# Performance work log

Measured on AMD Instinct MI355X. Metric: run time of the kernel, lower is better.

Reference implementation:

```python
import jax, jax.numpy as jnp
import numpy as np

NUM_HEADS = 6
KEY_DIM = 16
D_HEAD = 32  # attn_ratio(2) * key_dim(16)


def conv1x1_bn(x, W, scale, bias):
    # 1x1 conv (no bias) + folded BatchNorm (eval mode) as per-channel affine.
    y = jnp.einsum('oi,bihw->bohw', W, x)
    return y * scale[None, :, None, None] + bias[None, :, None, None]


def setup_inputs() -> dict:
    key = jax.random.key(0)
    ks = jax.random.split(key, 16)
    B, C, H, W = 4, 384, 48, 48
    dim_s = C // 4  # 96
    nh_kd = NUM_HEADS * KEY_DIM  # 96
    dh = NUM_HEADS * D_HEAD      # 192

    def w(k, o, i):
        return jax.random.normal(k, (o, i), dtype=jnp.float32) / np.sqrt(i)

    return {
        'xx': jax.random.normal(ks[0], (B, C, H, W), dtype=jnp.float32),
        'Wq': w(ks[1], nh_kd, dim_s),
        'q_scale': jax.random.uniform(ks[2], (nh_kd,), dtype=jnp.float32, minval=0.5, maxval=1.5),
        'q_bias': 0.1 * jax.random.normal(ks[3], (nh_kd,), dtype=jnp.float32),
        'Wk': w(ks[4], nh_kd, C),
        'k_scale': jax.random.uniform(ks[5], (nh_kd,), dtype=jnp.float32, minval=0.5, maxval=1.5),
        'k_bias': 0.1 * jax.random.normal(ks[6], (nh_kd,), dtype=jnp.float32),
        'Wv': w(ks[7], dh, C),
        'v_scale': jax.random.uniform(ks[8], (dh,), dtype=jnp.float32, minval=0.5, maxval=1.5),
        'v_bias': 0.1 * jax.random.normal(ks[9], (dh,), dtype=jnp.float32),
        'Wp': w(ks[10], dim_s, dh),
        'p_scale': jax.random.uniform(ks[11], (dim_s,), dtype=jnp.float32, minval=0.5, maxval=1.5),
        'p_bias': 0.1 * jax.random.normal(ks[12], (dim_s,), dtype=jnp.float32),
        'Wo': w(ks[13], C, dim_s),
        'o_scale': jax.random.uniform(ks[14], (C,), dtype=jnp.float32, minval=0.5, maxval=1.5),
        'o_bias': 0.1 * jax.random.normal(ks[15], (C,), dtype=jnp.float32),
    }


def reference(xx, Wq, q_scale, q_bias, Wk, k_scale, k_bias, Wv, v_scale, v_bias,
              Wp, p_scale, p_bias, Wo, o_scale, o_bias):
    B, C, H, W = xx.shape
    dim_s = C // 4
    N = H * W
    x = xx[:, 3 * dim_s:]  # last channel split -> query stream [B, dim_s, H, W]

    q = conv1x1_bn(x, Wq, q_scale, q_bias)                    # [B, nh_kd, H, W]
    q = q.reshape(B, NUM_HEADS, KEY_DIM, N).transpose(0, 1, 3, 2)  # [B,h,N,kd]
    k = conv1x1_bn(xx, Wk, k_scale, k_bias).reshape(B, NUM_HEADS, KEY_DIM, N)  # [B,h,kd,N]
    v = conv1x1_bn(xx, Wv, v_scale, v_bias).reshape(B, NUM_HEADS, D_HEAD, N)   # [B,h,d,N]

    # NOTE: original forward never applies key_dim**-0.5 scaling -- faithful to that.
    attn = jax.nn.softmax(jnp.einsum('bhnk,bhkm->bhnm', q, k), axis=-1)  # [B,h,N,N]
    out = jnp.einsum('bhnm,bhdm->bhdn', attn, v)                         # [B,h,d,N]
    out = out.reshape(B, NUM_HEADS * D_HEAD, H, W)

    out = conv1x1_bn(jax.nn.relu(out), Wp, p_scale, p_bias)  # [B, dim_s, H, W]
    xres = x + out  # drop_path=0 -> identity
    y = jax.nn.relu(conv1x1_bn(xres, Wo, o_scale, o_bias))   # [B, C, H, W]
    return y
```

## Files before the change

kernel.cpp:

```cpp
#include <hip/hip_runtime.h>
#include <hip/hip_bf16.h>
#include <math.h>

#define BB 4
#define CIN 384
#define NHD 6
#define KDIM 16
#define DHEAD 32
#define NPOS 2304
#define DIMS 96
#define DHTOT 192

constexpr size_t AL(size_t x) { return (x + 255) & ~(size_t)255; }
constexpr size_t B_SC1 = 0;
constexpr size_t B_BS1 = B_SC1 + 384 * 4;
constexpr size_t B_SC2 = B_BS1 + 384 * 4;
constexpr size_t B_BS2 = B_SC2 + 96 * 4;
constexpr size_t B_SC3 = B_BS2 + 96 * 4;
constexpr size_t B_BS3 = B_SC3 + 384 * 4;
constexpr size_t B_W1  = AL(B_BS3 + 384 * 4);
constexpr size_t B_W2  = AL(B_W1 + (size_t)384 * 384 * 2);
constexpr size_t B_W3  = AL(B_W2 + (size_t)96 * 192 * 2);
constexpr size_t B_XH  = AL(B_W3 + (size_t)384 * 96 * 2);
constexpr size_t B_XL  = AL(B_XH + (size_t)BB * NPOS * CIN * 2);
constexpr size_t B_Q   = AL(B_XL + (size_t)BB * NPOS * CIN * 2);
constexpr size_t B_K   = AL(B_Q + (size_t)BB * NHD * NPOS * KDIM * 2);
constexpr size_t B_V   = AL(B_K + (size_t)BB * NHD * NPOS * KDIM * 2);
constexpr size_t B_OP  = AL(B_V + (size_t)BB * NHD * DHEAD * NPOS * 2);
constexpr size_t B_MP  = AL(B_OP + (size_t)2 * BB * DHTOT * NPOS * 4);
constexpr size_t B_LP  = AL(B_MP + (size_t)2 * 24 * NPOS * 4);
constexpr size_t B_OBT = AL(B_LP + (size_t)2 * 24 * NPOS * 4);
constexpr size_t B_XRT = AL(B_OBT + (size_t)BB * NPOS * DHTOT * 2);

#define WS_F(off) ((float*)((char*)ws + (off)))
#define WS_U(off) ((ushort*)((char*)ws + (off)))

typedef __attribute__((ext_vector_type(8))) short bf16x8;
typedef __attribute__((ext_vector_type(16))) float f32x16;
typedef __attribute__((ext_vector_type(2))) int int2v;

__device__ inline ushort f2bf(float f) {
    __hip_bfloat16 h = __float2bfloat16(f);
    return *reinterpret_cast<ushort*>(&h);
}
__device__ inline float bf2f(ushort u) {
    uint x = (uint)u << 16;
    return __uint_as_float(x);
}
__device__ inline float exp2_fast(float x) {
    float r;
    asm volatile("v_exp_f32 %0, %1" : "=v"(r) : "v"(x));
    return r;
}
__device__ inline uint cvt_pk_bf16(float lo, float hi) {
    uint r;
    asm volatile("v_cvt_pk_bf16_f32 %0, %1, %2" : "=v"(r) : "v"(lo), "v"(hi));
    return r;
}
__device__ inline void phswap(uint& a, uint& b) {
    int2v r = __builtin_amdgcn_permlane32_swap((int)a, (int)b, false, false);
    a = (uint)r[0]; b = (uint)r[1];
}
__device__ inline float xhalf_max(float x) {
    uint a = __float_as_uint(x), b = a;
    phswap(a, b);
    return fmaxf(__uint_as_float(a), __uint_as_float(b));
}
__device__ inline float xhalf_add(float x) {
    uint a = __float_as_uint(x), b = a;
    phswap(a, b);
    return __uint_as_float(a) + __uint_as_float(b);
}

#define MFMA32(A, B, C) __builtin_amdgcn_mfma_f32_32x32x16_bf16(A, B, C, 0, 0, 0)
#define LOG2E 1.4426950408889634f

__global__ void prep_kernel(const float* Wq, const float* qs, const float* qb,
                            const float* Wk, const float* ks, const float* kb,
                            const float* Wv, const float* vs, const float* vb,
                            const float* Wp, const float* ps, const float* pb,
                            const float* Wo, const float* os_, const float* ob,
                            float* ws) {
    ushort* W1 = WS_U(B_W1);
    ushort* W2 = WS_U(B_W2);
    ushort* W3 = WS_U(B_W3);
    int idx = blockIdx.x * blockDim.x + threadIdx.x;
    int stride = gridDim.x * blockDim.x;
    for (int t = idx; t < 384 * 384; t += stride) {
        int o = t / 384, i = t % 384;
        float v;
        if (o < 96)       v = (i >= 288) ? Wq[o * 96 + (i - 288)] : 0.f;
        else if (o < 192) v = Wk[(o - 96) * 384 + i];
        else              v = Wv[(o - 192) * 384 + i];
        W1[t] = f2bf(v);
    }
    for (int t = idx; t < 96 * 192; t += stride) W2[t] = f2bf(Wp[t]);
    for (int t = idx; t < 384 * 96; t += stride) W3[t] = f2bf(Wo[t]);
    if (idx < 384) {
        float s, bv;
        if (idx < 96)       { s = qs[idx] * LOG2E; bv = qb[idx] * LOG2E; }
        else if (idx < 192) { s = ks[idx - 96];    bv = kb[idx - 96]; }
        else                { s = vs[idx - 192];   bv = vb[idx - 192]; }
        WS_F(B_SC1)[idx] = s;    WS_F(B_BS1)[idx] = bv;
        WS_F(B_SC3)[idx] = os_[idx]; WS_F(B_BS3)[idx] = ob[idx];
    }
    if (idx < 96) { WS_F(B_SC2)[idx] = ps[idx]; WS_F(B_BS2)[idx] = pb[idx]; }
}

__global__ __launch_bounds__(256) void xcvt(const float* __restrict__ xx, float* ws) {
    ushort* Xh = WS_U(B_XH);
    ushort* Xl = WS_U(B_XL);
    int nt = blockIdx.x, it = blockIdx.y, b = blockIdx.z;
    __shared__ ushort tileH[64][66];
    __shared__ ushort tileL[64][66];
    int t = threadIdx.x;
    int ir = t >> 4, nc = (t & 15) * 4;
    const float* src = xx + ((size_t)b * CIN + it * 64) * NPOS + nt * 64;
#pragma unroll
    for (int ii = 0; ii < 64; ii += 16) {
        float4 v = *(const float4*)&src[(size_t)(ii + ir) * NPOS + nc];
        float vv[4] = {v.x, v.y, v.z, v.w};
#pragma unroll
        for (int j = 0; j < 4; ++j) {
            ushort h = f2bf(vv[j]);
            tileH[ii + ir][nc + j] = h;
            tileL[ii + ir][nc + j] = f2bf(vv[j] - bf2f(h));
        }
    }
    __syncthreads();
    int nl = t >> 2, i16 = (t & 3) * 16;
    ushort tmpH[16], tmpL[16];
#pragma unroll
    for (int j = 0; j < 16; ++j) { tmpH[j] = tileH[i16 + j][nl]; tmpL[j] = tileL[i16 + j][nl]; }
    size_t doff = ((size_t)b * NPOS + nt * 64 + nl) * CIN + it * 64 + i16;
    *(bf16x8*)&Xh[doff]     = *(bf16x8*)&tmpH[0];
    *(bf16x8*)&Xh[doff + 8] = *(bf16x8*)&tmpH[8];
    *(bf16x8*)&Xl[doff]     = *(bf16x8*)&tmpL[0];
    *(bf16x8*)&Xl[doff + 8] = *(bf16x8*)&tmpL[8];
}

__global__ __launch_bounds__(256) void qkv_mfma(float* ws) {
    const ushort* W1 = WS_U(B_W1);
    const ushort* Xh = WS_U(B_XH);
    const ushort* Xl = WS_U(B_XL);
    const float* sc1 = WS_F(B_SC1);
    const float* bs1 = WS_F(B_BS1);
    ushort* Qb = WS_U(B_Q);
    ushort* Kb = WS_U(B_K);
    ushort* Vt = WS_U(B_V);

    int nt = blockIdx.x, ot = blockIdx.y, b = blockIdx.z;
    int wave = threadIdx.x >> 6, lane = threadIdx.x & 63;
    int l31 = lane & 31, hl = lane >> 5;
    int obase = ot * 64 + (wave >> 1) * 32;
    int nbase = nt * 64 + (wave & 1) * 32;

    const ushort* arow  = W1 + (size_t)(obase + l31) * CIN + hl * 8;
    size_t boff = ((size_t)b * NPOS + nbase + l31) * CIN + hl * 8;
    const ushort* browh = Xh + boff;
    f32x16 acc = {};
#pragma unroll
    for (int k0 = 0; k0 < 384; k0 += 16)
        acc = MFMA32(*(const bf16x8*)(arow + k0), *(const bf16x8*)(browh + k0), acc);
    if (obase < 192) {
        const ushort* browl = Xl + boff;
#pragma unroll
        for (int k0 = 0; k0 < 384; k0 += 16)
            acc = MFMA32(*(const bf16x8*)(arow + k0), *(const bf16x8*)(browl + k0), acc);
    }

    int n = nbase + l31;
    if (obase < 96) {
#pragma unroll
        for (int r = 0; r < 16; ++r) {
            int o = obase + (r & 3) + 8 * (r >> 2) + 4 * hl;
            float v = acc[r] * sc1[o] + bs1[o];
            int h = o >> 4, kk = o & 15;
            Qb[((size_t)(b * NHD + h) * NPOS + n) * KDIM + kk] = f2bf(v);
        }
    } else if (obase < 192) {
#pragma unroll
        for (int r = 0; r < 16; ++r) {
            int o = obase + (r & 3) + 8 * (r >> 2) + 4 * hl;
            float v = acc[r] * sc1[o] + bs1[o];
            int oo = o - 96;
            int h = oo >> 4, kk = oo & 15;
            Kb[((size_t)(b * NHD + h) * NPOS + n) * KDIM + kk] = f2bf(v);
        }
    } else {
#pragma unroll
        for (int r = 0; r < 16; ++r) {
            int o = obase + (r & 3) + 8 * (r >> 2) + 4 * hl;
            float v = acc[r] * sc1[o] + bs1[o];
            int oo = o - 192;
            int d = oo & 31, hh = oo >> 5;
            Vt[((size_t)(b * NHD + hh) * DHEAD + d) * NPOS + n] = f2bf(v);
        }
    }
}

__global__ __launch_bounds__(256) void attn_mfma(float* ws) {
    const ushort* Qb = WS_U(B_Q);
    const ushort* Kb = WS_U(B_K);
    const ushort* Vt = WS_U(B_V);
    float* Op = WS_F(B_OP);
    float* Mp = WS_F(B_MP);
    float* Lp = WS_F(B_LP);

    int qt = blockIdx.x;
    int bh = blockIdx.y;
    int ms = blockIdx.z;
    int wave = threadIdx.x >> 6, lane = threadIdx.x & 63;
    int l31 = lane & 31, hl = lane >> 5;
    int n0 = qt * 128 + wave * 32;
    int n = n0 + l31;

    bf16x8 qf = *(const bf16x8*)(Qb + ((size_t)bh * NPOS + n) * KDIM + hl * 8);
    const ushort* kbase = Kb + (size_t)bh * NPOS * KDIM;
    const ushort* vbase = Vt + (size_t)bh * DHEAD * NPOS + (size_t)l31 * NPOS;

    f32x16 oacc = (f32x16)0.0f;
    float m_run = -1e30f, l_run = 0.f;

    int mend = ms * 1152 + 1152;
    for (int m0 = ms * 1152; m0 < mend; m0 += 32) {
        bf16x8 kf = *(const bf16x8*)(kbase + (size_t)(m0 + l31) * KDIM + hl * 8);
        f32x16 s = MFMA32(kf, qf, (f32x16)0.0f);

        float pm = s[0];
#pragma unroll
        for (int r = 1; r < 16; ++r) pm = fmaxf(pm, s[r]);
        pm = xhalf_max(pm);

        if (__any(pm > m_run + 8.f)) {
            float newm = fmaxf(m_run, pm);
            float sc = exp2_fast(m_run - newm);
#pragma unroll
            for (int r = 0; r < 16; ++r) oacc[r] *= sc;
            l_run *= sc;
            m_run = newm;
        }

        float p[16], psum = 0.f;
#pragma unroll
        for (int r = 0; r < 16; ++r) { p[r] = exp2_fast(s[r] - m_run); psum += p[r]; }
        l_run += xhalf_add(psum);

        uint w[8];
#pragma unroll
        for (int j = 0; j < 8; ++j) w[j] = cvt_pk_bf16(p[2 * j], p[2 * j + 1]);
        phswap(w[0], w[2]);
        phswap(w[1], w[3]);
        phswap(w[4], w[6]);
        phswap(w[5], w[7]);

        bf16x8 pb0, pb1;
        ((uint*)&pb0)[0] = w[0]; ((uint*)&pb0)[1] = w[1];
        ((uint*)&pb0)[2] = w[2]; ((uint*)&pb0)[3] = w[3];
        ((uint*)&pb1)[0] = w[4]; ((uint*)&pb1)[1] = w[5];
        ((uint*)&pb1)[2] = w[6]; ((uint*)&pb1)[3] = w[7];

        bf16x8 va0 = *(const bf16x8*)(vbase + m0 + hl * 8);
        bf16x8 va1 = *(const bf16x8*)(vbase + m0 + 16 + hl * 8);
        oacc = MFMA32(va0, pb0, oacc);
        oacc = MFMA32(va1, pb1, oacc);
    }

    int b = bh / NHD, h = bh % NHD;
    float* obase = Op + ((size_t)(ms * BB + b) * DHTOT + h * DHEAD) * NPOS + n;
#pragma unroll
    for (int r = 0; r < 16; ++r) {
        int d = (r & 3) + 8 * (r >> 2) + 4 * hl;
        obase[(size_t)d * NPOS] = oacc[r];
    }
    Mp[(size_t)(ms * 24 + bh) * NPOS + n] = m_run;
    Lp[(size_t)(ms * 24 + bh) * NPOS + n] = l_run;
}

__global__ __launch_bounds__(256) void attn_combine(float* ws) {
    const float* Op = WS_F(B_OP);
    const float* Mp = WS_F(B_MP);
    const float* Lp = WS_F(B_LP);
    ushort* Obt = WS_U(B_OBT);

    int idx = blockIdx.x * 256 + threadIdx.x;
    int bh = idx / NPOS, n = idx % NPOS;
    int b = bh / NHD, h = bh % NHD;

    float m0 = Mp[(size_t)bh * NPOS + n];
    float m1 = Mp[(size_t)(24 + bh) * NPOS + n];
    float l0 = Lp[(size_t)bh * NPOS + n];
    float l1 = Lp[(size_t)(24 + bh) * NPOS + n];
    float gm = fmaxf(m0, m1);
    float w0 = exp2_fast(m0 - gm), w1 = exp2_fast(m1 - gm);
    float inv = 1.f / (l0 * w0 + l1 * w1);
    w0 *= inv; w1 *= inv;

    const float* p0 = Op + ((size_t)b * DHTOT + h * DHEAD) * NPOS + n;
    const float* p1 = Op + ((size_t)(BB + b) * DHTOT + h * DHEAD) * NPOS + n;
    ushort tmp[32];
#pragma unroll
    for (int d = 0; d < 32; ++d) {
        float v = p0[(size_t)d * NPOS] * w0 + p1[(size_t)d * NPOS] * w1;
        tmp[d] = f2bf(fmaxf(v, 0.f));
    }
    ushort* dst = Obt + ((size_t)b * NPOS + n) * DHTOT + h * DHEAD;
#pragma unroll
    for (int c = 0; c < 4; ++c) *(bf16x8*)&dst[c * 8] = *(bf16x8*)&tmp[c * 8];
}

__global__ __launch_bounds__(256) void pproj_mfma(const float* __restrict__ xx, float* ws) {
    const ushort* W2 = WS_U(B_W2);
    const ushort* Obt = WS_U(B_OBT);
    const float* sc2 = WS_F(B_SC2);
    const float* bs2 = WS_F(B_BS2);
    ushort* XRt = WS_U(B_XRT);

    int nt = blockIdx.x, ot = blockIdx.y, b = blockIdx.z;
    int wave = threadIdx.x >> 6, lane = threadIdx.x & 63;
    int l31 = lane & 31, hl = lane >> 5;
    int obase = ot * 32;
    int nbase = nt * 128 + wave * 32;

    const ushort* arow = W2 + (size_t)(obase + l31) * DHTOT + hl * 8;
    const ushort* brow = Obt + ((size_t)b * NPOS + nbase + l31) * DHTOT + hl * 8;
    f32x16 acc = {};
#pragma unroll
    for (int k0 = 0; k0 < 192; k0 += 16)
        acc = MFMA32(*(const bf16x8*)(arow + k0), *(const bf16x8*)(brow + k0), acc);

    int n = nbase + l31;
#pragma unroll
    for (int r = 0; r < 16; ++r) {
        int o = obase + (r & 3) + 8 * (r >> 2) + 4 * hl;
        float v = acc[r] * sc2[o] + bs2[o] + xx[((size_t)b * CIN + 288 + o) * NPOS + n];
        XRt[((size_t)b * NPOS + n) * DIMS + o] = f2bf(v);
    }
}

__global__ __launch_bounds__(256) void oproj_mfma(float* ws, float* __restrict__ y) {
    const ushort* W3 = WS_U(B_W3);
    const ushort* XRt = WS_U(B_XRT);
    const float* sc3 = WS_F(B_SC3);
    const float* bs3 = WS_F(B_BS3);

    int nt = blockIdx.x, ot = blockIdx.y, b = blockIdx.z;
    int wave = threadIdx.x >> 6, lane = threadIdx.x & 63;
    int l31 = lane & 31, hl = lane >> 5;
    int obase = ot * 64 + (wave >> 1) * 32;
    int nbase = nt * 64 + (wave & 1) * 32;

    const ushort* arow = W3 + (size_t)(obase + l31) * DIMS + hl * 8;
    const ushort* brow = XRt + ((size_t)b * NPOS + nbase + l31) * DIMS + hl * 8;
    f32x16 acc = {};
#pragma unroll
    for (int k0 = 0; k0 < 96; k0 += 16)
        acc = MFMA32(*(const bf16x8*)(arow + k0), *(const bf16x8*)(brow + k0), acc);

    int n = nbase + l31;
#pragma unroll
    for (int r = 0; r < 16; ++r) {
        int o = obase + (r & 3) + 8 * (r >> 2) + 4 * hl;
        float v = fmaxf(acc[r] * sc3[o] + bs3[o], 0.f);
        y[((size_t)b * CIN + o) * NPOS + n] = v;
    }
}

extern "C" void kernel_launch(void* const* d_in, const int* in_sizes, int n_in,
                              void* d_out, int out_size, void* d_ws, size_t ws_size,
                              hipStream_t stream) {
    const float* xx = (const float*)d_in[0];
    const float* Wq = (const float*)d_in[1];
    const float* qs = (const float*)d_in[2];
    const float* qb = (const float*)d_in[3];
    const float* Wk = (const float*)d_in[4];
    const float* ks = (const float*)d_in[5];
    const float* kb = (const float*)d_in[6];
    const float* Wv = (const float*)d_in[7];
    const float* vs = (const float*)d_in[8];
    const float* vb = (const float*)d_in[9];
    const float* Wp = (const float*)d_in[10];
    const float* ps = (const float*)d_in[11];
    const float* pb = (const float*)d_in[12];
    const float* Wo = (const float*)d_in[13];
    const float* os_ = (const float*)d_in[14];
    const float* ob = (const float*)d_in[15];
    float* ws = (float*)d_ws;
    float* y = (float*)d_out;

    prep_kernel<<<256, 256, 0, stream>>>(Wq, qs, qb, Wk, ks, kb, Wv, vs, vb,
                                         Wp, ps, pb, Wo, os_, ob, ws);
    xcvt<<<dim3(36, 6, BB), 256, 0, stream>>>(xx, ws);
    qkv_mfma<<<dim3(36, 6, BB), 256, 0, stream>>>(ws);
    attn_mfma<<<dim3(18, 24, 2), 256, 0, stream>>>(ws);
    attn_combine<<<216, 256, 0, stream>>>(ws);
    pproj_mfma<<<dim3(18, 3, BB), 256, 0, stream>>>(xx, ws);
    oproj_mfma<<<dim3(36, 6, BB), 256, 0, stream>>>(ws, y);
}
```

Baseline: 207.4 us.

## Split attention keys four ways, fuse prep into x conversion, vectorize Q/K stores

Raises the attention key-split factor from 2 to 4, so the grid grows to 1728 blocks and the combine kernel merges four partial results. Weight preparation moves into the x-conversion kernel, removing one launch. Q/K epilogue writes become packed 4-element stores, and the max and sum reductions are rebalanced into trees to shorten dependency chains. The price is larger partial-output buffers and more combine-stage traffic.

Result: no change. 204.2 us (-1.5%).

```diff
diff --git a/kernel.cpp b/kernel.cpp
--- a/kernel.cpp
+++ b/kernel.cpp
@@ -10,6 +10,7 @@
 #define NPOS 2304
 #define DIMS 96
 #define DHTOT 192
+#define MS 4
 
 constexpr size_t AL(size_t x) { return (x + 255) & ~(size_t)255; }
 constexpr size_t B_SC1 = 0;
@@ -27,9 +28,9 @@
 constexpr size_t B_K   = AL(B_Q + (size_t)BB * NHD * NPOS * KDIM * 2);
 constexpr size_t B_V   = AL(B_K + (size_t)BB * NHD * NPOS * KDIM * 2);
 constexpr size_t B_OP  = AL(B_V + (size_t)BB * NHD * DHEAD * NPOS * 2);
-constexpr size_t B_MP  = AL(B_OP + (size_t)2 * BB * DHTOT * NPOS * 4);
-constexpr size_t B_LP  = AL(B_MP + (size_t)2 * 24 * NPOS * 4);
-constexpr size_t B_OBT = AL(B_LP + (size_t)2 * 24 * NPOS * 4);
+constexpr size_t B_MP  = AL(B_OP + (size_t)MS * BB * DHTOT * NPOS * 4);
+constexpr size_t B_LP  = AL(B_MP + (size_t)MS * 24 * NPOS * 4);
+constexpr size_t B_OBT = AL(B_LP + (size_t)MS * 24 * NPOS * 4);
 constexpr size_t B_XRT = AL(B_OBT + (size_t)BB * NPOS * DHTOT * 2);
 
 #define WS_F(off) ((float*)((char*)ws + (off)))
@@ -57,6 +58,9 @@
     asm volatile("v_cvt_pk_bf16_f32 %0, %1, %2" : "=v"(r) : "v"(lo), "v"(hi));
     return r;
 }
+__device__ inline float fmax3(float a, float b, float c) {
+    return fmaxf(fmaxf(a, b), c);
+}
 __device__ inline void phswap(uint& a, uint& b) {
     int2v r = __builtin_amdgcn_permlane32_swap((int)a, (int)b, false, false);
     a = (uint)r[0]; b = (uint)r[1];
@@ -75,39 +79,13 @@
 #define MFMA32(A, B, C) __builtin_amdgcn_mfma_f32_32x32x16_bf16(A, B, C, 0, 0, 0)
 #define LOG2E 1.4426950408889634f
 
-__global__ void prep_kernel(const float* Wq, const float* qs, const float* qb,
+__global__ __launch_bounds__(256) void setup_kernel(const float* __restrict__ xx,
+                            const float* Wq, const float* qs, const float* qb,
                             const float* Wk, const float* ks, const float* kb,
                             const float* Wv, const float* vs, const float* vb,
                             const float* Wp, const float* ps, const float* pb,
                             const float* Wo, const float* os_, const float* ob,
                             float* ws) {
-    ushort* W1 = WS_U(B_W1);
-    ushort* W2 = WS_U(B_W2);
-    ushort* W3 = WS_U(B_W3);
-    int idx = blockIdx.x * blockDim.x + threadIdx.x;
-    int stride = gridDim.x * blockDim.x;
-    for (int t = idx; t < 384 * 384; t += stride) {
-        int o = t / 384, i = t % 384;
-        float v;
-        if (o < 96)       v = (i >= 288) ? Wq[o * 96 + (i - 288)] : 0.f;
-        else if (o < 192) v = Wk[(o - 96) * 384 + i];
-        else              v = Wv[(o - 192) * 384 + i];
-        W1[t] = f2bf(v);
-    }
-    for (int t = idx; t < 96 * 192; t += stride) W2[t] = f2bf(Wp[t]);
-    for (int t = idx; t < 384 * 96; t += stride) W3[t] = f2bf(Wo[t]);
-    if (idx < 384) {
-        float s, bv;
-        if (idx < 96)       { s = qs[idx] * LOG2E; bv = qb[idx] * LOG2E; }
-        else if (idx < 192) { s = ks[idx - 96];    bv = kb[idx - 96]; }
-        else                { s = vs[idx - 192];   bv = vb[idx - 192]; }
-        WS_F(B_SC1)[idx] = s;    WS_F(B_BS1)[idx] = bv;
-        WS_F(B_SC3)[idx] = os_[idx]; WS_F(B_BS3)[idx] = ob[idx];
-    }
-    if (idx < 96) { WS_F(B_SC2)[idx] = ps[idx]; WS_F(B_BS2)[idx] = pb[idx]; }
-}
-
-__global__ __launch_bounds__(256) void xcvt(const float* __restrict__ xx, float* ws) {
     ushort* Xh = WS_U(B_XH);
     ushort* Xl = WS_U(B_XL);
     int nt = blockIdx.x, it = blockIdx.y, b = blockIdx.z;
@@ -137,6 +115,35 @@
     *(bf16x8*)&Xh[doff + 8] = *(bf16x8*)&tmpH[8];
     *(bf16x8*)&Xl[doff]     = *(bf16x8*)&tmpL[0];
     *(bf16x8*)&Xl[doff + 8] = *(bf16x8*)&tmpL[8];
+
+    ushort* W1 = WS_U(B_W1);
+    ushort* W2 = WS_U(B_W2);
+    ushort* W3 = WS_U(B_W3);
+    int gid = (blockIdx.z * gridDim.y + blockIdx.y) * gridDim.x + blockIdx.x;
+    int idx = gid * 256 + t;
+    int stride = gridDim.x * gridDim.y * gridDim.z * 256;
+    for (int u = idx; u < 384 * 384; u += stride) {
+        int o = u / 384, i = u % 384;
+        float v;
+        if (o < 96)       v = (i >= 288) ? Wq[o * 96 + (i - 288)] : 0.f;
+        else if (o < 192) v = Wk[(o - 96) * 384 + i];
+        else              v = Wv[(o - 192) * 384 + i];
+        W1[u] = f2bf(v);
+    }
+    for (int u = idx; u < 96 * 192; u += stride) W2[u] = f2bf(Wp[u]);
+    for (int u = idx; u < 384 * 96; u += stride) W3[u] = f2bf(Wo[u]);
+    if (idx < 384) {
+        float s, bv;
+        if (idx < 96)       { s = qs[idx] * LOG2E; bv = qb[idx] * LOG2E; }
+        else if (idx < 192) { s = ks[idx - 96];    bv = kb[idx - 96]; }
+        else                { s = vs[idx - 192];   bv = vb[idx - 192]; }
+        WS_F(B_SC1)[idx] = s;    WS_F(B_BS1)[idx] = bv;
+        WS_F(B_SC3)[idx] = os_[idx]; WS_F(B_BS3)[idx] = ob[idx];
+    }
+    if (idx >= 256 * 256 && idx < 256 * 256 + 96) {
+        int j = idx - 256 * 256;
+        WS_F(B_SC2)[j] = ps[j]; WS_F(B_BS2)[j] = pb[j];
+    }
 }
 
 __global__ __launch_bounds__(256) void qkv_mfma(float* ws) {
@@ -170,22 +177,20 @@
     }
 
     int n = nbase + l31;
-    if (obase < 96) {
-#pragma unroll
-        for (int r = 0; r < 16; ++r) {
-            int o = obase + (r & 3) + 8 * (r >> 2) + 4 * hl;
-            float v = acc[r] * sc1[o] + bs1[o];
-            int h = o >> 4, kk = o & 15;
-            Qb[((size_t)(b * NHD + h) * NPOS + n) * KDIM + kk] = f2bf(v);
-        }
-    } else if (obase < 192) {
-#pragma unroll
-        for (int r = 0; r < 16; ++r) {
-            int o = obase + (r & 3) + 8 * (r >> 2) + 4 * hl;
-            float v = acc[r] * sc1[o] + bs1[o];
-            int oo = o - 96;
-            int h = oo >> 4, kk = oo & 15;
-            Kb[((size_t)(b * NHD + h) * NPOS + n) * KDIM + kk] = f2bf(v);
+    if (obase < 192) {
+        ushort* dst = (obase < 96) ? Qb : Kb;
+        int ob2 = (obase < 96) ? obase : obase - 96;
+#pragma unroll
+        for (int g = 0; g < 4; ++g) {
+            int od = ob2 + 8 * g + 4 * hl;
+            ushort4 pk;
+            float v0 = acc[4 * g + 0] * sc1[obase + 8 * g + 4 * hl + 0] + bs1[obase + 8 * g + 4 * hl + 0];
+            float v1 = acc[4 * g + 1] * sc1[obase + 8 * g + 4 * hl + 1] + bs1[obase + 8 * g + 4 * hl + 1];
+            float v2 = acc[4 * g + 2] * sc1[obase + 8 * g + 4 * hl + 2] + bs1[obase + 8 * g + 4 * hl + 2];
+            float v3 = acc[4 * g + 3] * sc1[obase + 8 * g + 4 * hl + 3] + bs1[obase + 8 * g + 4 * hl + 3];
+            pk.x = f2bf(v0); pk.y = f2bf(v1); pk.z = f2bf(v2); pk.w = f2bf(v3);
+            int h = od >> 4, kk = od & 15;
+            *(ushort4*)&dst[((size_t)(b * NHD + h) * NPOS + n) * KDIM + kk] = pk;
         }
     } else {
 #pragma unroll
@@ -222,14 +227,18 @@
     f32x16 oacc = (f32x16)0.0f;
     float m_run = -1e30f, l_run = 0.f;
 
-    int mend = ms * 1152 + 1152;
-    for (int m0 = ms * 1152; m0 < mend; m0 += 32) {
+    const int span = NPOS / MS;
+    int mstart = ms * span, mend = mstart + span;
+    for (int m0 = mstart; m0 < mend; m0 += 32) {
         bf16x8 kf = *(const bf16x8*)(kbase + (size_t)(m0 + l31) * KDIM + hl * 8);
         f32x16 s = MFMA32(kf, qf, (f32x16)0.0f);
 
-        float pm = s[0];
-#pragma unroll
-        for (int r = 1; r < 16; ++r) pm = fmaxf(pm, s[r]);
+        float t0 = fmax3(s[0], s[1], s[2]);
+        float t1 = fmax3(s[3], s[4], s[5]);
+        float t2 = fmax3(s[6], s[7], s[8]);
+        float t3 = fmax3(s[9], s[10], s[11]);
+        float t4 = fmax3(s[12], s[13], s[14]);
+        float pm = fmaxf(fmax3(t0, t1, t2), fmax3(t3, t4, s[15]));
         pm = xhalf_max(pm);
 
         if (__any(pm > m_run + 8.f)) {
@@ -241,10 +250,14 @@
             m_run = newm;
         }
 
-        float p[16], psum = 0.f;
-#pragma unroll
-        for (int r = 0; r < 16; ++r) { p[r] = exp2_fast(s[r] - m_run); psum += p[r]; }
-        l_run += xhalf_add(psum);
+        float p[16];
+#pragma unroll
+        for (int r = 0; r < 16; ++r) p[r] = exp2_fast(s[r] - m_run);
+        float a0 = (p[0] + p[1]) + (p[2] + p[3]);
+        float a1 = (p[4] + p[5]) + (p[6] + p[7]);
+        float a2 = (p[8] + p[9]) + (p[10] + p[11]);
+        float a3 = (p[12] + p[13]) + (p[14] + p[15]);
+        l_run += xhalf_add((a0 + a1) + (a2 + a3));
 
         uint w[8];
 #pragma unroll
@@ -287,21 +300,27 @@
     int bh = idx / NPOS, n = idx % NPOS;
     int b = bh / NHD, h = bh % NHD;
 
-    float m0 = Mp[(size_t)bh * NPOS + n];
-    float m1 = Mp[(size_t)(24 + bh) * NPOS + n];
-    float l0 = Lp[(size_t)bh * NPOS + n];
-    float l1 = Lp[(size_t)(24 + bh) * NPOS + n];
-    float gm = fmaxf(m0, m1);
-    float w0 = exp2_fast(m0 - gm), w1 = exp2_fast(m1 - gm);
-    float inv = 1.f / (l0 * w0 + l1 * w1);
-    w0 *= inv; w1 *= inv;
-
-    const float* p0 = Op + ((size_t)b * DHTOT + h * DHEAD) * NPOS + n;
-    const float* p1 = Op + ((size_t)(BB + b) * DHTOT + h * DHEAD) * NPOS + n;
+    float mv[MS], lv[MS];
+#pragma unroll
+    for (int s = 0; s < MS; ++s) {
+        mv[s] = Mp[(size_t)(s * 24 + bh) * NPOS + n];
+        lv[s] = Lp[(size_t)(s * 24 + bh) * NPOS + n];
+    }
+    float gm = fmaxf(fmaxf(mv[0], mv[1]), fmaxf(mv[2], mv[3]));
+    float wgt[MS], denom = 0.f;
+#pragma unroll
+    for (int s = 0; s < MS; ++s) { wgt[s] = exp2_fast(mv[s] - gm); denom += lv[s] * wgt[s]; }
+    float inv = 1.f / denom;
+#pragma unroll
+    for (int s = 0; s < MS; ++s) wgt[s] *= inv;
+
     ushort tmp[32];
 #pragma unroll
     for (int d = 0; d < 32; ++d) {
-        float v = p0[(size_t)d * NPOS] * w0 + p1[(size_t)d * NPOS] * w1;
+        float v = 0.f;
+#pragma unroll
+        for (int s = 0; s < MS; ++s)
+            v += Op[((size_t)(s * BB + b) * DHTOT + h * DHEAD + d) * NPOS + n] * wgt[s];
         tmp[d] = f2bf(fmaxf(v, 0.f));
     }
     ushort* dst = Obt + ((size_t)b * NPOS + n) * DHTOT + h * DHEAD;
@@ -388,11 +407,11 @@
     float* ws = (float*)d_ws;
     float* y = (float*)d_out;
 
-    prep_kernel<<<256, 256, 0, stream>>>(Wq, qs, qb, Wk, ks, kb, Wv, vs, vb,
-                                         Wp, ps, pb, Wo, os_, ob, ws);
-    xcvt<<<dim3(36, 6, BB), 256, 0, stream>>>(xx, ws);
+    setup_kernel<<<dim3(36, 6, BB), 256, 0, stream>>>(xx, Wq, qs, qb, Wk, ks, kb,
+                                                      Wv, vs, vb, Wp, ps, pb,
+                                                      Wo, os_, ob, ws);
     qkv_mfma<<<dim3(36, 6, BB), 256, 0, stream>>>(ws);
-    attn_mfma<<<dim3(18, 24, 2), 256, 0, stream>>>(ws);
+    attn_mfma<<<dim3(18, 24, MS), 256, 0, stream>>>(ws);
     attn_combine<<<216, 256, 0, stream>>>(ws);
     pproj_mfma<<<dim3(18, 3, BB), 256, 0, stream>>>(xx, ws);
     oproj_mfma<<<dim3(36, 6, BB), 256, 0, stream>>>(ws, y);
```
